# Kernel optimization log

Hardware: AMD Instinct MI355X
Metric: run time of the kernel (lower is better)

## Reference

```python
import jax, jax.numpy as jnp
import numpy as np

B, S, F_IN, F_OUT, K = 4, 4096, 64, 64, 32


def setup_inputs() -> dict:
    key = jax.random.key(0)
    k1, k2, k3 = jax.random.split(key, 3)
    X = jax.random.normal(k1, (B, S, F_IN), dtype=jnp.float32)
    M = jax.random.normal(k2, (B, S, K), dtype=jnp.float32)
    # xavier_uniform for weight: bound = sqrt(6/(fan_in+fan_out))
    bound = float(np.sqrt(6.0 / (F_IN + F_OUT)))
    weight = jax.random.uniform(k3, (F_IN, F_OUT), dtype=jnp.float32,
                                minval=-bound, maxval=bound)
    bias = jnp.zeros((F_OUT,), dtype=jnp.float32)
    return {"X": X, "M": M, "weight": weight, "bias": bias}


def reference(X, M, weight, bias):
    # similarity = softmax(relu(M M^T), axis=-1)  -> [B, S, S]
    sim_raw = jnp.einsum('bsk,btk->bst', M, M)
    sim = jax.nn.softmax(jax.nn.relu(sim_raw), axis=-1)
    # X W  -> [B, S, F_OUT]
    Xw = jnp.einsum('bsf,fo->bso', X, weight)
    # mode='add': (I + A) Xw = Xw + A @ Xw  (identity matmul folded)
    Z = Xw + jnp.einsum('bst,bto->bso', sim, Xw)
    Z = Z + bias
    # dropout is identity at inference (eval mode)
    return Z
```

## Files before the change

kernel.cpp:

```cpp
#include <hip/hip_runtime.h>
#include <cstdint>

#define BATCH  4
#define SLEN   4096
#define FDIM   64
#define KDIM   32
#define KSPLIT 4
#define CHUNK  (SLEN / KSPLIT)
#define NSTEP  (CHUNK / 64)
#define VSTRIDE 76

#define MSCALE 1.2011224087864498f

typedef __attribute__((ext_vector_type(8))) short bf16x8;
typedef __attribute__((ext_vector_type(4))) short bf16x4;
typedef __attribute__((ext_vector_type(4))) float f32x4;

#if __has_builtin(__builtin_amdgcn_exp2f)
#define EXP2(x) __builtin_amdgcn_exp2f(x)
#else
#define EXP2(x) exp2f(x)
#endif

static __device__ __forceinline__ short f2bf(float f) {
    union { float f; unsigned u; } v; v.f = f;
    unsigned r = v.u + 0x7fffu + ((v.u >> 16) & 1u);
    return (short)(r >> 16);
}
static __device__ __forceinline__ float bf2f(short s) {
    union { unsigned u; float f; } v;
    v.u = ((unsigned)(unsigned short)s) << 16;
    return v.f;
}
static __device__ __forceinline__ unsigned cvt_pk_bf16(float a, float b) {
    unsigned r;
    asm("v_cvt_pk_bf16_f32 %0, %1, %2" : "=v"(r) : "v"(a), "v"(b));
    return r;
}

__global__ __launch_bounds__(256) void prep(const float4* __restrict__ M4,
                                            ushort4* __restrict__ H4,
                                            ushort4* __restrict__ L4,
                                            const float4* __restrict__ X4,
                                            const float4* __restrict__ W4,
                                            float4* __restrict__ V4,
                                            short* __restrict__ Vt) {
    const int tid = threadIdx.x;
    const int blk = blockIdx.y * gridDim.x + blockIdx.x;
    if (blk < (BATCH * SLEN * KDIM) / (4 * 256)) {
        int i = blk * 256 + tid;
        float4 m = M4[i];
        float mx = m.x * MSCALE, my = m.y * MSCALE;
        float mz = m.z * MSCALE, mw = m.w * MSCALE;
        ushort4 h, l;
        h.x = (unsigned short)f2bf(mx); l.x = (unsigned short)f2bf(mx - bf2f((short)h.x));
        h.y = (unsigned short)f2bf(my); l.y = (unsigned short)f2bf(my - bf2f((short)h.y));
        h.z = (unsigned short)f2bf(mz); l.z = (unsigned short)f2bf(mz - bf2f((short)h.z));
        h.w = (unsigned short)f2bf(mw); l.w = (unsigned short)f2bf(mw - bf2f((short)h.w));
        H4[i] = h; L4[i] = l;
    }
    __shared__ float t[16][68];
    const int b  = blockIdx.y;
    const int s0 = blockIdx.x * 16;
    const int r  = tid >> 4;
    const int o4 = tid & 15;
    const float4* __restrict__ xr = X4 + ((size_t)b * SLEN + s0 + r) * (FDIM / 4);
    float4 acc = make_float4(0.f, 0.f, 0.f, 0.f);
#pragma unroll
    for (int f4 = 0; f4 < FDIM / 4; ++f4) {
        float4 x  = xr[f4];
        float4 w0 = W4[(f4 * 4 + 0) * 16 + o4];
        float4 w1 = W4[(f4 * 4 + 1) * 16 + o4];
        float4 w2 = W4[(f4 * 4 + 2) * 16 + o4];
        float4 w3 = W4[(f4 * 4 + 3) * 16 + o4];
        acc.x = fmaf(x.x, w0.x, fmaf(x.y, w1.x, fmaf(x.z, w2.x, fmaf(x.w, w3.x, acc.x))));
        acc.y = fmaf(x.x, w0.y, fmaf(x.y, w1.y, fmaf(x.z, w2.y, fmaf(x.w, w3.y, acc.y))));
        acc.z = fmaf(x.x, w0.z, fmaf(x.y, w1.z, fmaf(x.z, w2.z, fmaf(x.w, w3.z, acc.z))));
        acc.w = fmaf(x.x, w0.w, fmaf(x.y, w1.w, fmaf(x.z, w2.w, fmaf(x.w, w3.w, acc.w))));
    }
    V4[((size_t)b * SLEN + s0 + r) * 16 + o4] = acc;
    t[r][o4 * 4 + 0] = acc.x;
    t[r][o4 * 4 + 1] = acc.y;
    t[r][o4 * 4 + 2] = acc.z;
    t[r][o4 * 4 + 3] = acc.w;
    __syncthreads();
    const int c  = tid & 15;
    const int f0 = tid >> 4;
#pragma unroll
    for (int i2 = 0; i2 < 4; ++i2) {
        int f = f0 + i2 * 16;
        Vt[((size_t)b * FDIM + f) * SLEN + s0 + c] = f2bf(t[c][f]);
    }
}

__global__ __launch_bounds__(256, 2) void attn_mfma(const short* __restrict__ Mhi,
                                                    const short* __restrict__ Mlo,
                                                    const short* __restrict__ Vt,
                                                    float* __restrict__ accP,
                                                    float* __restrict__ lP) {
    const int bid  = blockIdx.x;
    const int slab = (bid & 7) + 8 * (bid >> 8);
    const int qblk = (bid >> 3) & 31;
    const int b    = slab >> 2;
    const int ks   = slab & 3;

    const int tid  = threadIdx.x;
    const int wave = tid >> 6;
    const int lane = tid & 63;
    const int col  = lane & 15;
    const int quad = lane >> 4;
    const int qbase = qblk * 128 + wave * 32;
    const int k0    = ks * CHUNK;

    const short* __restrict__ Mbh = Mhi + (size_t)b * SLEN * KDIM;
    const short* __restrict__ Mbl = Mlo + (size_t)b * SLEN * KDIM;
    const short* __restrict__ Vb  = Vt  + (size_t)b * FDIM * SLEN;

    __shared__ short khi[2][64 * 40];
    __shared__ short klo[2][64 * 40];
    __shared__ short vsh[2][64 * VSTRIDE];

    bf16x8 Qh[2], Ql[2];
#pragma unroll
    for (int tq = 0; tq < 2; ++tq) {
        int qo = (qbase + tq * 16 + col) * KDIM + quad * 8;
        Qh[tq] = *(const bf16x8*)(Mbh + qo);
        Ql[tq] = *(const bf16x8*)(Mbl + qo);
    }

    f32x4 accf[2][4];
#pragma unroll
    for (int tq = 0; tq < 2; ++tq)
#pragma unroll
        for (int fg = 0; fg < 4; ++fg) accf[tq][fg] = (f32x4){0.f, 0.f, 0.f, 0.f};
    float lacc[2] = {0.f, 0.f};

    const int krow = (tid & 127) >> 1;
    const int kp   = tid & 1;
    const int vrow = tid >> 2;
    const int vp   = tid & 3;
    const short* __restrict__ Msrc = (tid < 128) ? Mbh : Mbl;
    const int kg0 = krow * KDIM + (kp * 2 + 0) * 8;
    const int kg1 = krow * KDIM + (kp * 2 + 1) * 8;
    const int kl0 = krow * 40 + (kp * 2 + 0) * 8;
    const int kl1 = krow * 40 + (kp * 2 + 1) * 8;
    const int vl0 = vrow * VSTRIDE + (vp + 0) * 8;
    const int vl1 = vrow * VSTRIDE + (vp + 4) * 8;

    bf16x8 ksA = *(const bf16x8*)(Msrc + (size_t)k0 * KDIM + kg0);
    bf16x8 ksB = *(const bf16x8*)(Msrc + (size_t)k0 * KDIM + kg1);
    bf16x8 vsA = *(const bf16x8*)(Vb + (size_t)vrow * SLEN + k0 + (vp + 0) * 8);
    bf16x8 vsB = *(const bf16x8*)(Vb + (size_t)vrow * SLEN + k0 + (vp + 4) * 8);

#pragma unroll 1
    for (int step = 0; step < NSTEP; ++step) {
        const int cur = step & 1;
        short* __restrict__ kdst = (tid < 128) ? khi[cur] : klo[cur];
        *(bf16x8*)(kdst + kl0)     = ksA;
        *(bf16x8*)(kdst + kl1)     = ksB;
        *(bf16x8*)(vsh[cur] + vl0) = vsA;
        *(bf16x8*)(vsh[cur] + vl1) = vsB;
        if (step + 1 < NSTEP) {
            int kt = k0 + (step + 1) * 64;
            ksA = *(const bf16x8*)(Msrc + (size_t)kt * KDIM + kg0);
            ksB = *(const bf16x8*)(Msrc + (size_t)kt * KDIM + kg1);
            vsA = *(const bf16x8*)(Vb + (size_t)vrow * SLEN + kt + (vp + 0) * 8);
            vsB = *(const bf16x8*)(Vb + (size_t)vrow * SLEN + kt + (vp + 4) * 8);
        }
        asm volatile("s_waitcnt lgkmcnt(0)" ::: "memory");
        __builtin_amdgcn_s_barrier();
        __builtin_amdgcn_sched_barrier(0);

        const short* __restrict__ kh = khi[cur];
        const short* __restrict__ kl = klo[cur];
        const short* __restrict__ vv = vsh[cur];

        bf16x8 Kh[4], Kl[4];
#pragma unroll
        for (int t = 0; t < 4; ++t) {
            Kh[t] = *(const bf16x8*)(kh + (t * 16 + col) * 40 + quad * 8);
            Kl[t] = *(const bf16x8*)(kl + (t * 16 + col) * 40 + quad * 8);
        }
        bf16x8 Vg[4][2];
#pragma unroll
        for (int fg = 0; fg < 4; ++fg)
#pragma unroll
            for (int g = 0; g < 2; ++g) {
                const short* vp_ = vv + (fg * 16 + col) * VSTRIDE + g * 32 + quad * 4;
                bf16x4 vlo = *(const bf16x4*)(vp_);
                bf16x4 vhi = *(const bf16x4*)(vp_ + 16);
                Vg[fg][g] = __builtin_shufflevector(vlo, vhi, 0, 1, 2, 3, 4, 5, 6, 7);
            }

        __builtin_amdgcn_s_setprio(1);
#pragma unroll
        for (int tq = 0; tq < 2; ++tq) {
            f32x4 c[4];
#pragma unroll
            for (int t = 0; t < 4; ++t) {
                f32x4 z = (f32x4){0.f, 0.f, 0.f, 0.f};
                c[t] = __builtin_amdgcn_mfma_f32_16x16x32_bf16(Kh[t], Ql[tq], z, 0, 0, 0);
                c[t] = __builtin_amdgcn_mfma_f32_16x16x32_bf16(Kl[t], Qh[tq], c[t], 0, 0, 0);
                c[t] = __builtin_amdgcn_mfma_f32_16x16x32_bf16(Kh[t], Qh[tq], c[t], 0, 0, 0);
            }
            float e[16];
#pragma unroll
            for (int t = 0; t < 4; ++t) {
                e[t * 4 + 0] = EXP2(fmaxf(c[t][0], 0.f));
                e[t * 4 + 1] = EXP2(fmaxf(c[t][1], 0.f));
                e[t * 4 + 2] = EXP2(fmaxf(c[t][2], 0.f));
                e[t * 4 + 3] = EXP2(fmaxf(c[t][3], 0.f));
            }
            lacc[tq] += (((e[0] + e[1]) + (e[2] + e[3])) + ((e[4] + e[5]) + (e[6] + e[7])))
                      + (((e[8] + e[9]) + (e[10] + e[11])) + ((e[12] + e[13]) + (e[14] + e[15])));

            union { unsigned u[4]; bf16x8 v; } pa0, pa1;
            pa0.u[0] = cvt_pk_bf16(e[0],  e[1]);
            pa0.u[1] = cvt_pk_bf16(e[2],  e[3]);
            pa0.u[2] = cvt_pk_bf16(e[4],  e[5]);
            pa0.u[3] = cvt_pk_bf16(e[6],  e[7]);
            pa1.u[0] = cvt_pk_bf16(e[8],  e[9]);
            pa1.u[1] = cvt_pk_bf16(e[10], e[11]);
            pa1.u[2] = cvt_pk_bf16(e[12], e[13]);
            pa1.u[3] = cvt_pk_bf16(e[14], e[15]);

#pragma unroll
            for (int fg = 0; fg < 4; ++fg) {
                accf[tq][fg] = __builtin_amdgcn_mfma_f32_16x16x32_bf16(
                    pa0.v, Vg[fg][0], accf[tq][fg], 0, 0, 0);
                accf[tq][fg] = __builtin_amdgcn_mfma_f32_16x16x32_bf16(
                    pa1.v, Vg[fg][1], accf[tq][fg], 0, 0, 0);
            }
        }
        __builtin_amdgcn_s_setprio(0);
    }

#pragma unroll
    for (int tq = 0; tq < 2; ++tq) {
#pragma unroll
        for (int j = 0; j < 4; ++j) {
            int q = qbase + tq * 16 + quad * 4 + j;
            size_t base = ((size_t)b * SLEN + q) * KSPLIT + ks;
            float* __restrict__ op = accP + base * FDIM;
#pragma unroll
            for (int fg = 0; fg < 4; ++fg)
                op[fg * 16 + col] = accf[tq][fg][j];
        }
        float lv = lacc[tq];
        lv += __shfl_xor(lv, 16);
        lv += __shfl_xor(lv, 32);
        if (quad == 0) {
            int q = qbase + tq * 16 + col;
            lP[((size_t)b * SLEN + q) * KSPLIT + ks] = lv;
        }
    }
}

__global__ __launch_bounds__(256) void combine_kernel(const float4* __restrict__ V4,
                                                      const float4* __restrict__ accP4,
                                                      const float4* __restrict__ lP4,
                                                      const float4* __restrict__ bias4,
                                                      float4* __restrict__ out4) {
    int i  = blockIdx.x * 256 + threadIdx.x;
    int o4 = i & 15;
    int row = i >> 4;
    float nx = 0.f, ny = 0.f, nz = 0.f, nw = 0.f;
#pragma unroll
    for (int k = 0; k < KSPLIT; ++k) {
        float4 a = accP4[((size_t)row * KSPLIT + k) * 16 + o4];
        nx += a.x; ny += a.y; nz += a.z; nw += a.w;
    }
    float4 l = lP4[row];
    float den = (l.x + l.y) + (l.z + l.w);
    float r = 1.f / den;
    float4 v = V4[i];
    float4 bb = bias4[o4];
    float4 o;
    o.x = v.x + nx * r + bb.x;
    o.y = v.y + ny * r + bb.y;
    o.z = v.z + nz * r + bb.z;
    o.w = v.w + nw * r + bb.w;
    out4[i] = o;
}

extern "C" void kernel_launch(void* const* d_in, const int* in_sizes, int n_in,
                              void* d_out, int out_size, void* d_ws, size_t ws_size,
                              hipStream_t stream) {
    const float* X    = (const float*)d_in[0];
    const float* M    = (const float*)d_in[1];
    const float* W    = (const float*)d_in[2];
    const float* bias = (const float*)d_in[3];
    float* out = (float*)d_out;

    const size_t vElems = (size_t)BATCH * SLEN * FDIM;
    const size_t mElems = (size_t)BATCH * SLEN * KDIM;
    const size_t rows   = (size_t)BATCH * SLEN;

    float* Vf   = (float*)d_ws;
    float* accP = Vf + vElems;
    float* lP   = accP + vElems * KSPLIT;
    short* Mhi  = (short*)(lP + rows * KSPLIT);
    short* Mlo  = Mhi + mElems;
    short* Vt   = Mlo + mElems;

    prep<<<dim3(SLEN / 16, BATCH), 256, 0, stream>>>(
        (const float4*)M, (ushort4*)Mhi, (ushort4*)Mlo,
        (const float4*)X, (const float4*)W, (float4*)Vf, Vt);

    attn_mfma<<<dim3((SLEN / 128) * BATCH * KSPLIT), 256, 0, stream>>>(
        Mhi, Mlo, Vt, accP, lP);

    combine_kernel<<<(int)(vElems / 1024), 256, 0, stream>>>(
        (const float4*)Vf, (const float4*)accP, (const float4*)lP,
        (const float4*)bias, (float4*)out);
}
```

Before: 109.0 us.

## Fuse split-K combine into attention kernel via last-block atomic counter

Removes the separate combine kernel launch. Each attention block writes its partial accumulators in a per-query-block layout, then bumps an atomic counter. The last of the KSPLIT blocks for a query block reduces the partials, applies normalization, residual and bias, and writes the output. This saves one kernel launch and the extra pass over the partial buffer, at the cost of fences, an atomic per block, and a serialized tail on the last-arriving block.

```diff
diff --git a/kernel.cpp b/kernel.cpp
--- a/kernel.cpp
+++ b/kernel.cpp
@@ -9,6 +9,7 @@
 #define CHUNK  (SLEN / KSPLIT)
 #define NSTEP  (CHUNK / 64)
 #define VSTRIDE 76
+#define NQBLK  (SLEN / 128)
 
 #define MSCALE 1.2011224087864498f
 
@@ -44,9 +45,11 @@
                                             const float4* __restrict__ X4,
                                             const float4* __restrict__ W4,
                                             float4* __restrict__ V4,
-                                            short* __restrict__ Vt) {
+                                            short* __restrict__ Vt,
+                                            unsigned* __restrict__ cnt) {
     const int tid = threadIdx.x;
     const int blk = blockIdx.y * gridDim.x + blockIdx.x;
+    if (blk == 0 && tid < BATCH * NQBLK) cnt[tid] = 0;
     if (blk < (BATCH * SLEN * KDIM) / (4 * 256)) {
         int i = blk * 256 + tid;
         float4 m = M4[i];
@@ -97,12 +100,17 @@
                                                     const short* __restrict__ Mlo,
                                                     const short* __restrict__ Vt,
                                                     float* __restrict__ accP,
-                                                    float* __restrict__ lP) {
+                                                    float* __restrict__ lP,
+                                                    unsigned* __restrict__ cnt,
+                                                    const float4* __restrict__ V4,
+                                                    const float4* __restrict__ bias4,
+                                                    float4* __restrict__ out4) {
     const int bid  = blockIdx.x;
     const int slab = (bid & 7) + 8 * (bid >> 8);
     const int qblk = (bid >> 3) & 31;
     const int b    = slab >> 2;
     const int ks   = slab & 3;
+    const int pbq  = b * NQBLK + qblk;
 
     const int tid  = threadIdx.x;
     const int wave = tid >> 6;
@@ -119,6 +127,7 @@
     __shared__ short khi[2][64 * 40];
     __shared__ short klo[2][64 * 40];
     __shared__ short vsh[2][64 * VSTRIDE];
+    __shared__ int lastflag;
 
     bf16x8 Qh[2], Ql[2];
 #pragma unroll
@@ -235,13 +244,13 @@
         __builtin_amdgcn_s_setprio(0);
     }
 
+    float* __restrict__ myP = accP + ((size_t)pbq * KSPLIT + ks) * (128 * 64);
 #pragma unroll
     for (int tq = 0; tq < 2; ++tq) {
 #pragma unroll
         for (int j = 0; j < 4; ++j) {
-            int q = qbase + tq * 16 + quad * 4 + j;
-            size_t base = ((size_t)b * SLEN + q) * KSPLIT + ks;
-            float* __restrict__ op = accP + base * FDIM;
+            int ql = wave * 32 + tq * 16 + quad * 4 + j;
+            float* __restrict__ op = myP + ql * 64;
 #pragma unroll
             for (int fg = 0; fg < 4; ++fg)
                 op[fg * 16 + col] = accf[tq][fg][j];
@@ -250,37 +259,51 @@
         lv += __shfl_xor(lv, 16);
         lv += __shfl_xor(lv, 32);
         if (quad == 0) {
-            int q = qbase + tq * 16 + col;
-            lP[((size_t)b * SLEN + q) * KSPLIT + ks] = lv;
-        }
-    }
-}
-
-__global__ __launch_bounds__(256) void combine_kernel(const float4* __restrict__ V4,
-                                                      const float4* __restrict__ accP4,
-                                                      const float4* __restrict__ lP4,
-                                                      const float4* __restrict__ bias4,
-                                                      float4* __restrict__ out4) {
-    int i  = blockIdx.x * 256 + threadIdx.x;
-    int o4 = i & 15;
-    int row = i >> 4;
-    float nx = 0.f, ny = 0.f, nz = 0.f, nw = 0.f;
-#pragma unroll
-    for (int k = 0; k < KSPLIT; ++k) {
-        float4 a = accP4[((size_t)row * KSPLIT + k) * 16 + o4];
-        nx += a.x; ny += a.y; nz += a.z; nw += a.w;
-    }
-    float4 l = lP4[row];
-    float den = (l.x + l.y) + (l.z + l.w);
-    float r = 1.f / den;
-    float4 v = V4[i];
-    float4 bb = bias4[o4];
-    float4 o;
-    o.x = v.x + nx * r + bb.x;
-    o.y = v.y + ny * r + bb.y;
-    o.z = v.z + nz * r + bb.z;
-    o.w = v.w + nw * r + bb.w;
-    out4[i] = o;
+            int ql = wave * 32 + tq * 16 + col;
+            lP[((size_t)pbq * 128 + ql) * KSPLIT + ks] = lv;
+        }
+    }
+
+    __threadfence();
+    __syncthreads();
+    if (tid == 0) {
+        unsigned prev = __hip_atomic_fetch_add(&cnt[pbq], 1u,
+                                               __ATOMIC_ACQ_REL,
+                                               __HIP_MEMORY_SCOPE_AGENT);
+        lastflag = (prev == KSPLIT - 1);
+    }
+    __syncthreads();
+    if (lastflag) {
+        __threadfence();
+        const float4* __restrict__ Pp  = (const float4*)(accP + (size_t)pbq * KSPLIT * (128 * 64));
+        const float4* __restrict__ lp4 = (const float4*)(lP + (size_t)pbq * 128 * KSPLIT);
+#pragma unroll
+        for (int t = 0; t < 8; ++t) {
+            int i  = t * 256 + tid;
+            int o4 = i & 15;
+            int ql = i >> 4;
+            float4 l = lp4[ql];
+            float r = 1.f / ((l.x + l.y) + (l.z + l.w));
+            float nx = 0.f, ny = 0.f, nz = 0.f, nw = 0.f;
+#pragma unroll
+            for (int k2 = 0; k2 < KSPLIT; ++k2) {
+                float4 a = Pp[((size_t)k2 * 128 + ql) * 16 + o4];
+                nx += a.x; ny += a.y; nz += a.z; nw += a.w;
+            }
+            size_t gi = ((size_t)b * SLEN + qblk * 128 + ql) * 16 + o4;
+            float4 v  = V4[gi];
+            float4 bb = bias4[o4];
+            float4 o;
+            o.x = v.x + nx * r + bb.x;
+            o.y = v.y + ny * r + bb.y;
+            o.z = v.z + nz * r + bb.z;
+            o.w = v.w + nw * r + bb.w;
+            out4[gi] = o;
+        }
+        if (tid == 0)
+            __hip_atomic_store(&cnt[pbq], 0u, __ATOMIC_RELAXED,
+                               __HIP_MEMORY_SCOPE_AGENT);
+    }
 }
 
 extern "C" void kernel_launch(void* const* d_in, const int* in_sizes, int n_in,
@@ -296,21 +319,19 @@
     const size_t mElems = (size_t)BATCH * SLEN * KDIM;
     const size_t rows   = (size_t)BATCH * SLEN;
 
-    float* Vf   = (float*)d_ws;
-    float* accP = Vf + vElems;
-    float* lP   = accP + vElems * KSPLIT;
-    short* Mhi  = (short*)(lP + rows * KSPLIT);
-    short* Mlo  = Mhi + mElems;
-    short* Vt   = Mlo + mElems;
+    float*    Vf   = (float*)d_ws;
+    float*    accP = Vf + vElems;
+    float*    lP   = accP + vElems * KSPLIT;
+    unsigned* cnt  = (unsigned*)(lP + rows * KSPLIT);
+    short*    Mhi  = (short*)(cnt + 128);
+    short*    Mlo  = Mhi + mElems;
+    short*    Vt   = Mlo + mElems;
 
     prep<<<dim3(SLEN / 16, BATCH), 256, 0, stream>>>(
         (const float4*)M, (ushort4*)Mhi, (ushort4*)Mlo,
-        (const float4*)X, (const float4*)W, (float4*)Vf, Vt);
+        (const float4*)X, (const float4*)W, (float4*)Vf, Vt, cnt);
 
     attn_mfma<<<dim3((SLEN / 128) * BATCH * KSPLIT), 256, 0, stream>>>(
-        Mhi, Mlo, Vt, accP, lP);
-
-    combine_kernel<<<(int)(vElems / 1024), 256, 0, stream>>>(
-        (const float4*)Vf, (const float4*)accP, (const float4*)lP,
-        (const float4*)bias, (float4*)out);
-}
+        Mhi, Mlo, Vt, accP, lP, cnt,
+        (const float4*)Vf, (const float4*)bias, (float4*)out);
+}
```

Measured after the change: 211.6 us. 1.94x slower.
